# Kernel tuning notes

Hardware: AMD Instinct MI355X
Metric: run time of the kernel (lower is better)

The kernel has to match this reference:

```python
import jax, jax.numpy as jnp
import numpy as np

ALPHA = 0.1
EPS = 1e-8


def _segment_mean_std(feats, idx, num_segments):
    # feats: (N, C), idx: (N,) int -> mean/std per segment, torch.std is unbiased (ddof=1)
    ones = jnp.ones((feats.shape[0],), feats.dtype)
    cnt = jax.ops.segment_sum(ones, idx, num_segments=num_segments)  # (B,)
    ssum = jax.ops.segment_sum(feats, idx, num_segments=num_segments)  # (B, C)
    mean = ssum / cnt[:, None]
    diff = feats - mean[idx]
    var = jax.ops.segment_sum(diff * diff, idx, num_segments=num_segments) / (cnt[:, None] - 1.0)
    std = jnp.sqrt(jnp.maximum(var, 0.0)) + EPS
    return mean, std


def _adain(content_feats, style_feats, content_batch_indices, style_batch_indices, num_batches):
    c_mean, c_std = _segment_mean_std(content_feats, content_batch_indices, num_batches)
    s_mean, s_std = _segment_mean_std(style_feats, style_batch_indices, num_batches)
    # sequential EMA of global stats across batch ids (globals start as first batch's style stats)
    g0 = jnp.concatenate([s_mean[:1], s_std[:1]], axis=0)  # (2, C)
    rest = jnp.stack([s_mean[1:], s_std[1:]], axis=1)  # (B-1, 2, C)

    def step(g, s):
        g_new = (1.0 - ALPHA) * g + ALPHA * s
        return g_new, g_new

    _, g_rest = jax.lax.scan(step, g0, rest)
    g_all = jnp.concatenate([g0[None], g_rest], axis=0)  # (B, 2, C)
    g_mean, g_std = g_all[:, 0], g_all[:, 1]  # (B, C) each
    # per-row gather + normalize (each batch uses globals AFTER its own update)
    ci = content_batch_indices
    return g_std[ci] * (content_feats - c_mean[ci]) / c_std[ci] + g_mean[ci]


def setup_inputs() -> dict:
    key = jax.random.key(0)
    k1, k2, k3, k4 = jax.random.split(key, 4)
    N_c, N_s, C, B = 1000000, 250000, 64, 16
    return {
        "content_feats": jax.random.normal(k1, (N_c, C), dtype=jnp.float32),
        "style_feats": jax.random.normal(k2, (N_s, C), dtype=jnp.float32),
        "content_batch_indices": jax.random.randint(k3, (N_c,), 0, B, dtype=jnp.int32),
        "style_batch_indices": jax.random.randint(k4, (N_s,), 0, B, dtype=jnp.int32),
        "num_batches": B,
    }


def reference(content_feats, style_feats, content_batch_indices, style_batch_indices, num_batches):
    return _adain(content_feats, style_feats, content_batch_indices, style_batch_indices, num_batches)
```

## Files before the change

### kernel.cpp

```cpp
#include <hip/hip_runtime.h>


#define NB 16
#define NC 64
#define NREP 16
#define CBLKS 1024
#define SBLKS 256

typedef float fvec4 __attribute__((ext_vector_type(4)));
typedef float f32x4 __attribute__((ext_vector_type(4)));
typedef short bf16x8 __attribute__((ext_vector_type(8)));

#define WS_CPART 0
#define WS_SPART (NREP * 2048)
#define WS_CCNT  (2 * NREP * 2048)
#define WS_SCNT  (WS_CCNT + NREP * NB)
#define WS_SCALE (WS_SCNT + NREP * NB)
#define WS_BIAS  (WS_SCALE + 1024)
#define WS_ZERO_FLOATS WS_SCALE

__device__ __forceinline__ unsigned cvtpk(float lo, float hi)
{
    unsigned r;
    asm("v_cvt_pk_bf16_f32 %0, %1, %2" : "=v"(r) : "v"(lo), "v"(hi));
    return r;
}

__device__ __forceinline__ void reduce_body(
    const float* __restrict__ feats, const int* __restrict__ idx, int nrows,
    float* __restrict__ part, float* __restrict__ cntp,
    int blk, int nblk, int tid, float* lsum )
{
    const int lane = tid & 63;
    const int wv   = tid >> 6;
    const int half = lane >> 4;
    const int sub  = lane & 15;

    f32x4 accS[4], accQ[4];
    #pragma unroll
    for (int q = 0; q < 4; ++q) { accS[q] = f32x4{0,0,0,0}; accQ[q] = f32x4{0,0,0,0}; }
    int cnti = 0;

    const int ntiles = (nrows + 31) >> 5;
    const int W   = nblk * 4;
    const int tpw = (ntiles + W - 1) / W;
    const int w   = blk * 4 + wv;
    int t0 = w * tpw;
    int t1 = t0 + tpw; if (t1 > ntiles) t1 = ntiles;

    for (int t = t0; t < t1; ++t) {
        const int rb = t << 5;
        const int rl = rb + (lane & 31);
        const int vidx = (rl < nrows) ? idx[rl] : -1;

        #pragma unroll
        for (int b = 0; b < NB; ++b) {
            const unsigned long long m = __ballot(vidx == b) & 0xFFFFFFFFull;
            cnti += (lane == b) ? (int)__popcll(m) : 0;
        }

        union { unsigned w[4]; bf16x8 v; } A;
        const int kb4 = half * 32;
        #pragma unroll
        for (int i = 0; i < 4; ++i) {
            const int k0 = __builtin_amdgcn_ds_bpermute(kb4 + 8 * i,     vidx);
            const int k1 = __builtin_amdgcn_ds_bpermute(kb4 + 8 * i + 4, vidx);
            const unsigned lo = (k0 == sub) ? 0x3F80u     : 0u;
            const unsigned hi = (k1 == sub) ? 0x3F800000u : 0u;
            A.w[i] = lo | hi;
        }

        float xv[4][8];
        #pragma unroll
        for (int q = 0; q < 4; ++q) {
            #pragma unroll
            for (int j = 0; j < 8; ++j) {
                int r = rb + half * 8 + j;
                if (r > nrows - 1) r = nrows - 1;
                xv[q][j] = feats[(size_t)r * NC + q * 16 + sub];
            }
        }

        #pragma unroll
        for (int q = 0; q < 4; ++q) {
            union { unsigned w[4]; bf16x8 v; } Bs, Bq;
            #pragma unroll
            for (int i = 0; i < 4; ++i) {
                const float a0 = xv[q][2 * i], a1 = xv[q][2 * i + 1];
                Bs.w[i] = cvtpk(a0, a1);
                Bq.w[i] = cvtpk(a0 * a0, a1 * a1);
            }
            accS[q] = __builtin_amdgcn_mfma_f32_16x16x32_bf16(A.v, Bs.v, accS[q], 0, 0, 0);
            accQ[q] = __builtin_amdgcn_mfma_f32_16x16x32_bf16(A.v, Bq.v, accQ[q], 0, 0, 0);
        }
    }

    float* my = lsum + wv * 2048;
    #pragma unroll
    for (int q = 0; q < 4; ++q) {
        #pragma unroll
        for (int i = 0; i < 4; ++i) {
            const int m = half * 4 + i;
            my[m * NC + q * 16 + sub]        = accS[q][i];
            my[1024 + m * NC + q * 16 + sub] = accQ[q][i];
        }
    }
    __syncthreads();
    float* dst = part + (blk & (NREP - 1)) * 2048;
    for (int i = tid; i < 2048; i += 256)
        atomicAdd(&dst[i], lsum[i] + lsum[2048 + i] + lsum[4096 + i] + lsum[6144 + i]);
    if (lane < NB)
        atomicAdd(&cntp[(blk & (NREP - 1)) * NB + lane], (float)cnti);
}

__global__ __launch_bounds__(256) void reduce_stats(
    const float* __restrict__ content, const int* __restrict__ ci, int Nc,
    const float* __restrict__ style,   const int* __restrict__ si, int Ns,
    float* __restrict__ ws)
{
    __shared__ float lsum[4 * 2048];
    if (blockIdx.x < CBLKS)
        reduce_body(content, ci, Nc, ws + WS_CPART, ws + WS_CCNT,
                    blockIdx.x, CBLKS, threadIdx.x, lsum);
    else
        reduce_body(style, si, Ns, ws + WS_SPART, ws + WS_SCNT,
                    blockIdx.x - CBLKS, SBLKS, threadIdx.x, lsum);
}

__global__ void finalize_kernel(float* __restrict__ ws)
{
    if (threadIdx.x >= NC) return;
    const int c = threadIdx.x;
    const float* c_part = ws + WS_CPART;
    const float* s_part = ws + WS_SPART;
    const float* c_cntp = ws + WS_CCNT;
    const float* s_cntp = ws + WS_SCNT;
    float* scale = ws + WS_SCALE;
    float* bias  = ws + WS_BIAS;

    float gm = 0.f, gs = 0.f;
    for (int b = 0; b < NB; ++b) {
        float csum = 0.f, csq = 0.f, ssum = 0.f, ssq = 0.f, ccnt = 0.f, scnt = 0.f;
        #pragma unroll
        for (int rep = 0; rep < NREP; ++rep) {
            csum += c_part[rep * 2048 + b * NC + c];
            csq  += c_part[rep * 2048 + 1024 + b * NC + c];
            ssum += s_part[rep * 2048 + b * NC + c];
            ssq  += s_part[rep * 2048 + 1024 + b * NC + c];
            ccnt += c_cntp[rep * NB + b];
            scnt += s_cntp[rep * NB + b];
        }
        const float smean = ssum / scnt;
        const float svar  = (ssq - scnt * smean * smean) / (scnt - 1.0f);
        const float sstd  = sqrtf(fmaxf(svar, 0.f)) + 1e-8f;
        if (b == 0) { gm = smean; gs = sstd; }
        else        { gm = 0.9f * gm + 0.1f * smean; gs = 0.9f * gs + 0.1f * sstd; }
        const float cmean = csum / ccnt;
        const float cvar  = (csq - ccnt * cmean * cmean) / (ccnt - 1.0f);
        const float cstd  = sqrtf(fmaxf(cvar, 0.f)) + 1e-8f;
        const float sc = gs / cstd;
        scale[b * NC + c] = sc;
        bias [b * NC + c] = gm - sc * cmean;
    }
}

__global__ __launch_bounds__(256) void apply_kernel(
    const float* __restrict__ content, const int* __restrict__ ci, int Nc,
    const float* __restrict__ ws, fvec4* __restrict__ out4)
{
    __shared__ fvec4 s_sc[NB * 17];
    __shared__ fvec4 s_bi[NB * 17];
    const fvec4* scale4 = (const fvec4*)(ws + WS_SCALE);
    const fvec4* bias4  = (const fvec4*)(ws + WS_BIAS);
    for (int i = threadIdx.x; i < NB * 16; i += 256) {
        const int b = i >> 4, c4 = i & 15;
        s_sc[b * 17 + c4] = scale4[i];
        s_bi[b * 17 + c4] = bias4[i];
    }
    __syncthreads();

    const fvec4* feats4 = (const fvec4*)content;
    const int total4 = Nc * 16;
    const int stride = gridDim.x * 256;
    for (int i = blockIdx.x * 256 + threadIdx.x; i < total4; i += stride) {
        const int r  = i >> 4;
        const int c4 = i & 15;
        const int b  = ci[r];
        const fvec4 v  = feats4[i];
        const fvec4 sc = s_sc[b * 17 + c4];
        const fvec4 bi = s_bi[b * 17 + c4];
        fvec4 o;
        o.x = fmaf(sc.x, v.x, bi.x);
        o.y = fmaf(sc.y, v.y, bi.y);
        o.z = fmaf(sc.z, v.z, bi.z);
        o.w = fmaf(sc.w, v.w, bi.w);
        __builtin_nontemporal_store(o, &out4[i]);
    }
}

extern "C" void kernel_launch(void* const* d_in, const int* in_sizes, int n_in,
                              void* d_out, int out_size, void* d_ws, size_t ws_size,
                              hipStream_t stream)
{
    const float* content = (const float*)d_in[0];
    const float* style   = (const float*)d_in[1];
    const int*   ci      = (const int*)d_in[2];
    const int*   si      = (const int*)d_in[3];

    const int Nc = in_sizes[0] / NC;
    const int Ns = in_sizes[1] / NC;

    float* ws = (float*)d_ws;
    (void)hipMemsetAsync(ws, 0, WS_ZERO_FLOATS * sizeof(float), stream);

    reduce_stats<<<CBLKS + SBLKS, 256, 0, stream>>>(content, ci, Nc, style, si, Ns, ws);
    finalize_kernel<<<1, 64, 0, stream>>>(ws);
    apply_kernel<<<2048, 256, 0, stream>>>(content, ci, Nc, ws, (fvec4*)d_out);
}
```

Measured before the change: 184.4 us.

## Stage reduce tiles through LDS with async global_load_lds and split channels across waves

The stats reduction now has each block process its tiles cooperatively: the four waves split the 64 channels, so each wave handles 16 columns of a 32-row tile. Tile data is prefetched into shared memory with global_load_lds, double-stepped with two barriers per tile, and the next tile's indices are loaded ahead. The block count is raised and the final LDS reduction is shortened since each wave owns a disjoint column slice. In exchange it adds two __syncthreads per tile and serialises the load-to-compute handoff through a single LDS buffer, so any overlap between load and compute is limited.

```diff
diff --git a/kernel.cpp b/kernel.cpp
--- a/kernel.cpp
+++ b/kernel.cpp
@@ -4,8 +4,8 @@
 #define NB 16
 #define NC 64
 #define NREP 16
-#define CBLKS 1024
-#define SBLKS 256
+#define CBLKS 1638
+#define SBLKS 410
 
 typedef float fvec4 __attribute__((ext_vector_type(4)));
 typedef float f32x4 __attribute__((ext_vector_type(4)));
@@ -26,37 +26,63 @@
     return r;
 }
 
+__device__ __forceinline__ void gload16(const float* g, float* l)
+{
+    __builtin_amdgcn_global_load_lds(
+        (const __attribute__((address_space(1))) void*)g,
+        (__attribute__((address_space(3))) void*)l, 16, 0, 0);
+}
+
 __device__ __forceinline__ void reduce_body(
     const float* __restrict__ feats, const int* __restrict__ idx, int nrows,
     float* __restrict__ part, float* __restrict__ cntp,
-    int blk, int nblk, int tid, float* lsum )
+    int blk, int nblk, int tid, float* buf , float* lsum )
 {
     const int lane = tid & 63;
     const int wv   = tid >> 6;
     const int half = lane >> 4;
     const int sub  = lane & 15;
 
-    f32x4 accS[4], accQ[4];
-    #pragma unroll
-    for (int q = 0; q < 4; ++q) { accS[q] = f32x4{0,0,0,0}; accQ[q] = f32x4{0,0,0,0}; }
+    const int ntiles = (nrows + 31) >> 5;
+    const int tpb = (ntiles + nblk - 1) / nblk;
+    const int t0 = blk * tpb;
+    const int t1 = (t0 + tpb < ntiles) ? (t0 + tpb) : ntiles;
+
+    f32x4 accS = {0, 0, 0, 0}, accQ = {0, 0, 0, 0};
     int cnti = 0;
 
-    const int ntiles = (nrows + 31) >> 5;
-    const int W   = nblk * 4;
-    const int tpw = (ntiles + W - 1) / W;
-    const int w   = blk * 4 + wv;
-    int t0 = w * tpw;
-    int t1 = t0 + tpw; if (t1 > ntiles) t1 = ntiles;
+    const int i0 = 2 * wv, i1 = 2 * wv + 1;
+    const int srow0 = i0 * 4 + (sub >> 2) * 0 + (lane >> 4);
+    const int scol  = (lane & 15) * 4;
+
+    int vidx_next = -1;
+    if (t0 < t1) {
+        const int rl = (t0 << 5) + (lane & 31);
+        vidx_next = (rl < nrows) ? idx[rl] : -1;
+        {
+            const int rb = t0 << 5;
+            int ra = rb + i0 * 4 + (lane >> 4); if (ra > nrows - 1) ra = nrows - 1;
+            int rbx = rb + i1 * 4 + (lane >> 4); if (rbx > nrows - 1) rbx = nrows - 1;
+            gload16(feats + (size_t)ra * NC + (lane & 15) * 4, buf + i0 * 256);
+            gload16(feats + (size_t)rbx * NC + (lane & 15) * 4, buf + i1 * 256);
+        }
+    }
 
     for (int t = t0; t < t1; ++t) {
-        const int rb = t << 5;
-        const int rl = rb + (lane & 31);
-        const int vidx = (rl < nrows) ? idx[rl] : -1;
-
-        #pragma unroll
-        for (int b = 0; b < NB; ++b) {
-            const unsigned long long m = __ballot(vidx == b) & 0xFFFFFFFFull;
-            cnti += (lane == b) ? (int)__popcll(m) : 0;
+        __syncthreads();
+        const int vidx = vidx_next;
+
+        if (t + 1 < t1) {
+            const int rl = ((t + 1) << 5) + (lane & 31);
+            vidx_next = (rl < nrows) ? idx[rl] : -1;
+        }
+
+        if (wv == 0) {
+            #pragma unroll
+            for (int b = 0; b < NB; ++b) {
+                const unsigned long long m = __ballot(vidx == b) & 0xFFFFFFFFull;
+                cnti += (lane == b) ? (int)__popcll(m) : 0;
+            }
         }
 
         union { unsigned w[4]; bf16x8 v; } A;
@@ -70,46 +96,44 @@
             A.w[i] = lo | hi;
         }
 
-        float xv[4][8];
-        #pragma unroll
-        for (int q = 0; q < 4; ++q) {
-            #pragma unroll
-            for (int j = 0; j < 8; ++j) {
-                int r = rb + half * 8 + j;
-                if (r > nrows - 1) r = nrows - 1;
-                xv[q][j] = feats[(size_t)r * NC + q * 16 + sub];
-            }
-        }
-
-        #pragma unroll
-        for (int q = 0; q < 4; ++q) {
-            union { unsigned w[4]; bf16x8 v; } Bs, Bq;
-            #pragma unroll
-            for (int i = 0; i < 4; ++i) {
-                const float a0 = xv[q][2 * i], a1 = xv[q][2 * i + 1];
-                Bs.w[i] = cvtpk(a0, a1);
-                Bq.w[i] = cvtpk(a0 * a0, a1 * a1);
-            }
-            accS[q] = __builtin_amdgcn_mfma_f32_16x16x32_bf16(A.v, Bs.v, accS[q], 0, 0, 0);
-            accQ[q] = __builtin_amdgcn_mfma_f32_16x16x32_bf16(A.v, Bq.v, accQ[q], 0, 0, 0);
-        }
-    }
-
-    float* my = lsum + wv * 2048;
+        float xv[8];
+        #pragma unroll
+        for (int j = 0; j < 8; ++j)
+            xv[j] = buf[(half * 8 + j) * NC + wv * 16 + sub];
+
+        union { unsigned w[4]; bf16x8 v; } Bs, Bq;
+        #pragma unroll
+        for (int i = 0; i < 4; ++i) {
+            const float a0 = xv[2 * i], a1 = xv[2 * i + 1];
+            Bs.w[i] = cvtpk(a0, a1);
+            Bq.w[i] = cvtpk(a0 * a0, a1 * a1);
+        }
+
+        __syncthreads();
+
+        if (t + 1 < t1) {
+            const int rb = (t + 1) << 5;
+            int ra = rb + i0 * 4 + (lane >> 4); if (ra > nrows - 1) ra = nrows - 1;
+            int rbx = rb + i1 * 4 + (lane >> 4); if (rbx > nrows - 1) rbx = nrows - 1;
+            gload16(feats + (size_t)ra * NC + (lane & 15) * 4, buf + i0 * 256);
+            gload16(feats + (size_t)rbx * NC + (lane & 15) * 4, buf + i1 * 256);
+        }
+
+        accS = __builtin_amdgcn_mfma_f32_16x16x32_bf16(A.v, Bs.v, accS, 0, 0, 0);
+        accQ = __builtin_amdgcn_mfma_f32_16x16x32_bf16(A.v, Bq.v, accQ, 0, 0, 0);
+    }
+
     #pragma unroll
-    for (int q = 0; q < 4; ++q) {
-        #pragma unroll
-        for (int i = 0; i < 4; ++i) {
-            const int m = half * 4 + i;
-            my[m * NC + q * 16 + sub]        = accS[q][i];
-            my[1024 + m * NC + q * 16 + sub] = accQ[q][i];
-        }
+    for (int i = 0; i < 4; ++i) {
+        const int m = half * 4 + i;
+        lsum[m * NC + wv * 16 + sub]        = accS[i];
+        lsum[1024 + m * NC + wv * 16 + sub] = accQ[i];
     }
     __syncthreads();
     float* dst = part + (blk & (NREP - 1)) * 2048;
     for (int i = tid; i < 2048; i += 256)
-        atomicAdd(&dst[i], lsum[i] + lsum[2048 + i] + lsum[4096 + i] + lsum[6144 + i]);
-    if (lane < NB)
+        atomicAdd(&dst[i], lsum[i]);
+    if (wv == 0 && lane < NB)
         atomicAdd(&cntp[(blk & (NREP - 1)) * NB + lane], (float)cnti);
 }
 
@@ -118,13 +142,14 @@
     const float* __restrict__ style,   const int* __restrict__ si, int Ns,
     float* __restrict__ ws)
 {
-    __shared__ float lsum[4 * 2048];
+    __shared__ float buf[2048];
+    __shared__ float lsum[2048];
     if (blockIdx.x < CBLKS)
         reduce_body(content, ci, Nc, ws + WS_CPART, ws + WS_CCNT,
-                    blockIdx.x, CBLKS, threadIdx.x, lsum);
+                    blockIdx.x, CBLKS, threadIdx.x, buf, lsum);
     else
         reduce_body(style, si, Ns, ws + WS_SPART, ws + WS_SCNT,
-                    blockIdx.x - CBLKS, SBLKS, threadIdx.x, lsum);
+                    blockIdx.x - CBLKS, SBLKS, threadIdx.x, buf, lsum);
 }
 
 __global__ void finalize_kernel(float* __restrict__ ws)
```

New measurement: 186.4 us, median of 2. About the same (+1.1%).

## Split channel quarters across waves in reduction; reverse apply traversal order

Applied to the files above, without the earlier changes.

The reduction kernel gives each of the four waves in a block one 16-channel quarter of the same 32-row tile, replacing the per-wave contiguous tile ranges that covered all 64 channels. This removes the 4x shared-memory partials and the cross-wave sum, cuts accumulator registers, and strides tiles across blocks, with block counts raised to fill more CUs. The apply kernel now walks its grid-stride loop in reverse, likely so it first touches the most recently read content data still in cache. The risks are that all four waves reload the same index row per tile, and that more blocks issue more atomics onto the partial buffers.

```diff
diff --git a/kernel.cpp b/kernel.cpp
--- a/kernel.cpp
+++ b/kernel.cpp
@@ -4,8 +4,8 @@
 #define NB 16
 #define NC 64
 #define NREP 16
-#define CBLKS 1024
-#define SBLKS 256
+#define CBLKS 1638
+#define SBLKS 410
 
 typedef float fvec4 __attribute__((ext_vector_type(4)));
 typedef float f32x4 __attribute__((ext_vector_type(4)));
@@ -36,27 +36,22 @@
     const int half = lane >> 4;
     const int sub  = lane & 15;
 
-    f32x4 accS[4], accQ[4];
-    #pragma unroll
-    for (int q = 0; q < 4; ++q) { accS[q] = f32x4{0,0,0,0}; accQ[q] = f32x4{0,0,0,0}; }
+    f32x4 accS = {0, 0, 0, 0}, accQ = {0, 0, 0, 0};
     int cnti = 0;
 
     const int ntiles = (nrows + 31) >> 5;
-    const int W   = nblk * 4;
-    const int tpw = (ntiles + W - 1) / W;
-    const int w   = blk * 4 + wv;
-    int t0 = w * tpw;
-    int t1 = t0 + tpw; if (t1 > ntiles) t1 = ntiles;
-
-    for (int t = t0; t < t1; ++t) {
+
+    for (int t = blk; t < ntiles; t += nblk) {
         const int rb = t << 5;
         const int rl = rb + (lane & 31);
         const int vidx = (rl < nrows) ? idx[rl] : -1;
 
-        #pragma unroll
-        for (int b = 0; b < NB; ++b) {
-            const unsigned long long m = __ballot(vidx == b) & 0xFFFFFFFFull;
-            cnti += (lane == b) ? (int)__popcll(m) : 0;
+        if (wv == 0) {
+            #pragma unroll
+            for (int b = 0; b < NB; ++b) {
+                const unsigned long long m = __ballot(vidx == b) & 0xFFFFFFFFull;
+                cnti += (lane == b) ? (int)__popcll(m) : 0;
+            }
         }
 
         union { unsigned w[4]; bf16x8 v; } A;
@@ -70,46 +65,37 @@
             A.w[i] = lo | hi;
         }
 
-        float xv[4][8];
-        #pragma unroll
-        for (int q = 0; q < 4; ++q) {
-            #pragma unroll
-            for (int j = 0; j < 8; ++j) {
-                int r = rb + half * 8 + j;
-                if (r > nrows - 1) r = nrows - 1;
-                xv[q][j] = feats[(size_t)r * NC + q * 16 + sub];
-            }
-        }
-
-        #pragma unroll
-        for (int q = 0; q < 4; ++q) {
-            union { unsigned w[4]; bf16x8 v; } Bs, Bq;
-            #pragma unroll
-            for (int i = 0; i < 4; ++i) {
-                const float a0 = xv[q][2 * i], a1 = xv[q][2 * i + 1];
-                Bs.w[i] = cvtpk(a0, a1);
-                Bq.w[i] = cvtpk(a0 * a0, a1 * a1);
-            }
-            accS[q] = __builtin_amdgcn_mfma_f32_16x16x32_bf16(A.v, Bs.v, accS[q], 0, 0, 0);
-            accQ[q] = __builtin_amdgcn_mfma_f32_16x16x32_bf16(A.v, Bq.v, accQ[q], 0, 0, 0);
-        }
-    }
-
-    float* my = lsum + wv * 2048;
+        float xv[8];
+        #pragma unroll
+        for (int j = 0; j < 8; ++j) {
+            int r = rb + half * 8 + j;
+            if (r > nrows - 1) r = nrows - 1;
+            xv[j] = feats[(size_t)r * NC + wv * 16 + sub];
+        }
+
+        union { unsigned w[4]; bf16x8 v; } Bs, Bq;
+        #pragma unroll
+        for (int i = 0; i < 4; ++i) {
+            const float a0 = xv[2 * i], a1 = xv[2 * i + 1];
+            Bs.w[i] = cvtpk(a0, a1);
+            Bq.w[i] = cvtpk(a0 * a0, a1 * a1);
+        }
+
+        accS = __builtin_amdgcn_mfma_f32_16x16x32_bf16(A.v, Bs.v, accS, 0, 0, 0);
+        accQ = __builtin_amdgcn_mfma_f32_16x16x32_bf16(A.v, Bq.v, accQ, 0, 0, 0);
+    }
+
     #pragma unroll
-    for (int q = 0; q < 4; ++q) {
-        #pragma unroll
-        for (int i = 0; i < 4; ++i) {
-            const int m = half * 4 + i;
-            my[m * NC + q * 16 + sub]        = accS[q][i];
-            my[1024 + m * NC + q * 16 + sub] = accQ[q][i];
-        }
+    for (int i = 0; i < 4; ++i) {
+        const int m = half * 4 + i;
+        lsum[m * NC + wv * 16 + sub]        = accS[i];
+        lsum[1024 + m * NC + wv * 16 + sub] = accQ[i];
     }
     __syncthreads();
     float* dst = part + (blk & (NREP - 1)) * 2048;
     for (int i = tid; i < 2048; i += 256)
-        atomicAdd(&dst[i], lsum[i] + lsum[2048 + i] + lsum[4096 + i] + lsum[6144 + i]);
-    if (lane < NB)
+        atomicAdd(&dst[i], lsum[i]);
+    if (wv == 0 && lane < NB)
         atomicAdd(&cntp[(blk & (NREP - 1)) * NB + lane], (float)cnti);
 }
 
@@ -118,7 +104,7 @@
     const float* __restrict__ style,   const int* __restrict__ si, int Ns,
     float* __restrict__ ws)
 {
-    __shared__ float lsum[4 * 2048];
+    __shared__ float lsum[2048];
     if (blockIdx.x < CBLKS)
         reduce_body(content, ci, Nc, ws + WS_CPART, ws + WS_CCNT,
                     blockIdx.x, CBLKS, threadIdx.x, lsum);
@@ -182,7 +168,10 @@
     const fvec4* feats4 = (const fvec4*)content;
     const int total4 = Nc * 16;
     const int stride = gridDim.x * 256;
-    for (int i = blockIdx.x * 256 + threadIdx.x; i < total4; i += stride) {
+    const int nsteps = (total4 + stride - 1) / stride;
+    for (int s = nsteps - 1; s >= 0; --s) {
+        const int i = s * stride + blockIdx.x * 256 + threadIdx.x;
+        if (i >= total4) continue;
         const int r  = i >> 4;
         const int c4 = i & 15;
         const int b  = ci[r];
```

Result: slower. 200.9 us (+9.0%).
